# Kernel optimization log

Hardware: AMD Instinct MI355X
Metric: run time of the kernel (lower is better)

## Reference

```python
import jax, jax.numpy as jnp
import numpy as np

H = 12          # num_attention_heads
D = 768         # hidden_size
R = 4           # channel_shrink_ratio
DH = D // H     # 64, attention_head_size
DL = D // R     # 192, layout hidden size
DHL = DH // R   # 16, layout head size
NEG = jnp.finfo(jnp.float32).min


def setup_inputs() -> dict:
    key = jax.random.key(0)
    ks = jax.random.split(key, 16)
    B, S = 8, 1024
    s = 0.02
    inp = {
        "hidden_states": jax.random.normal(ks[0], (B, S, D), jnp.float32),
        "layout_hidden_states": jax.random.normal(ks[1], (B, S, DL), jnp.float32),
        "attention_mask": jnp.ones((B, S), jnp.float32),
        "Wq": jax.random.normal(ks[2], (D, D), jnp.float32) * s,
        "bq": jnp.zeros((D,), jnp.float32),
        "Wk": jax.random.normal(ks[3], (D, D), jnp.float32) * s,
        "bk": jnp.zeros((D,), jnp.float32),
        "Wv": jax.random.normal(ks[4], (D, D), jnp.float32) * s,
        "bv": jnp.zeros((D,), jnp.float32),
        "Wlq": jax.random.normal(ks[5], (DL, DL), jnp.float32) * s,
        "blq": jnp.zeros((DL,), jnp.float32),
        "Wlk": jax.random.normal(ks[6], (DL, DL), jnp.float32) * s,
        "blk": jnp.zeros((DL,), jnp.float32),
        "Wlv": jax.random.normal(ks[7], (DL, DL), jnp.float32) * s,
        "blv": jnp.zeros((DL,), jnp.float32),
    }
    return inp


def _heads(x, hd):
    # [B,S,H*hd] -> [B,H,S,hd]
    B, S, _ = x.shape
    return x.reshape(B, S, H, hd).transpose(0, 2, 1, 3)


def reference(hidden_states, layout_hidden_states, attention_mask,
              Wq, bq, Wk, bk, Wv, bv, Wlq, blq, Wlk, blk, Wlv, blv):
    B, S, _ = hidden_states.shape
    q = _heads(hidden_states @ Wq.T + bq, DH)
    k = _heads(hidden_states @ Wk.T + bk, DH)
    v = _heads(hidden_states @ Wv.T + bv, DH)
    lq = _heads(layout_hidden_states @ Wlq.T + blq, DHL)
    lk = _heads(layout_hidden_states @ Wlk.T + blk, DHL)
    lv = _heads(layout_hidden_states @ Wlv.T + blv, DHL)

    scores = jnp.einsum('bhqd,bhkd->bhqk', q, k) / jnp.sqrt(jnp.float32(DH))
    lscores = jnp.einsum('bhqd,bhkd->bhqk', lq, lk) / jnp.sqrt(jnp.float32(DHL))
    fused = scores + lscores  # cross-added scores (same for both streams)

    bias = (1.0 - attention_mask)[:, None, None, :] * NEG  # [B,1,1,S]
    fused = fused + bias

    probs = jax.nn.softmax(fused, axis=-1)   # dropout disabled (p=0)

    ctx = jnp.einsum('bhqk,bhkd->bhqd', probs, v)
    ctx = ctx.transpose(0, 2, 1, 3).reshape(B, S, D)
    lctx = jnp.einsum('bhqk,bhkd->bhqd', probs, lv)
    lctx = lctx.transpose(0, 2, 1, 3).reshape(B, S, DL)
    return ctx, lctx, probs
```

## Files before the change

### kernel.cpp

```cpp
#include <hip/hip_runtime.h>

#define NH   12
#define SEQ  1024
#define NB   8
#define DCAT 96
#define DV   80

typedef __attribute__((ext_vector_type(8))) short  bf16x8;
typedef __attribute__((ext_vector_type(4))) float  f32x4;
typedef __attribute__((ext_vector_type(4))) unsigned short u16x4;

static __device__ __forceinline__ unsigned short f2bf(float x) {
    unsigned int u = __float_as_uint(x);
    u += 0x7fffu + ((u >> 16) & 1u);
    return (unsigned short)(u >> 16);
}
static __device__ __forceinline__ f32x4 fzero() {
    f32x4 z; z[0]=0.f; z[1]=0.f; z[2]=0.f; z[3]=0.f; return z;
}
static __device__ __forceinline__ unsigned int cvtpk(float lo, float hi) {
    unsigned int r;
    asm("v_cvt_pk_bf16_f32 %0, %1, %2" : "=v"(r) : "v"(lo), "v"(hi));
    return r;
}
// ... 34 lines not shown
    o[0] = f2bf(v[0]); o[1] = f2bf(v[1]); o[2] = f2bf(v[2]); o[3] = f2bf(v[3]);
    ((u16x4*)dst)[off] = o;
}

__global__ __launch_bounds__(256) void proj_gemm(
    const unsigned short* __restrict__ A,
    const unsigned short* __restrict__ Bw,
    const float* __restrict__ b0, const float* __restrict__ b1, const float* __restrict__ b2,
    unsigned short* __restrict__ Qc, unsigned short* __restrict__ Kc, unsigned short* __restrict__ VT,
    int K, int Ntot, int variant)
{
    __shared__ __align__(16) unsigned short As[4096];
    __shared__ __align__(16) unsigned short Bs[4096];
    const int tid = threadIdx.x, w = tid >> 6, lane = tid & 63;
    const int g = lane >> 4, c = lane & 15;
    const int m0 = blockIdx.x * 128, n0 = blockIdx.y * 128;
    const int wr = w >> 1, wc = w & 1;
    const int srow = lane >> 2, scol = (lane & 3) * 8;

    f32x4 acc[4][4];
    #pragma unroll
    for (int m = 0; m < 4; m++)
        #pragma unroll
        for (int n = 0; n < 4; n++) acc[m][n] = fzero();

    const int ch0 = w * 2, ch1 = w * 2 + 1;
    const size_t arow0 = (size_t)(m0 + ch0 * 16 + srow) * K + scol;
    const size_t arow1 = (size_t)(m0 + ch1 * 16 + srow) * K + scol;
    int bn0 = n0 + ch0 * 16 + srow; if (bn0 >= Ntot) bn0 = Ntot - 1;
    int bn1 = n0 + ch1 * 16 + srow; if (bn1 >= Ntot) bn1 = Ntot - 1;
    const size_t brow0 = (size_t)bn0 * K + scol;
    const size_t brow1 = (size_t)bn1 * K + scol;

    for (int k0 = 0; k0 < K; k0 += 32) {
        __syncthreads();
        GLDS16(A  + arow0 + k0, As + ch0 * 512);
        GLDS16(A  + arow1 + k0, As + ch1 * 512);
        GLDS16(Bw + brow0 + k0, Bs + ch0 * 512);
        GLDS16(Bw + brow1 + k0, Bs + ch1 * 512);
        __syncthreads();
        bf16x8 af[4], bfr[4];
        #pragma unroll
        for (int m = 0; m < 4; m++) af[m]  = *(const bf16x8*)&As[(wr*64 + m*16 + c)*32 + g*8];
        #pragma unroll
        for (int n = 0; n < 4; n++) bfr[n] = *(const bf16x8*)&Bs[(wc*64 + n*16 + c)*32 + g*8];
        #pragma unroll
        for (int m = 0; m < 4; m++)
            #pragma unroll
            for (int n = 0; n < 4; n++)
                acc[m][n] = __builtin_amdgcn_mfma_f32_16x16x32_bf16(af[m], bfr[n], acc[m][n], 0, 0, 0);
    }

    const int b_ = m0 >> 10;
    #pragma unroll
    for (int nf = 0; nf < 4; nf++) {
        int n = n0 + wc * 64 + nf * 16 + c;
        if (n >= Ntot) continue;
        int seg, nn;
        if (variant == 0) { seg = (n >= 1536) ? 2 : ((n >= 768) ? 1 : 0); nn = n - seg * 768; }
        else              { seg = (n >= 384)  ? 2 : ((n >= 192) ? 1 : 0); nn = n - seg * 192; }
        const float* bp = (seg == 0) ? b0 : ((seg == 1) ? b1 : b2);
        float bv = bp[nn];
        float scale = (seg == 0) ? (variant ? 0.25f : 0.125f) : 1.0f;
        int h, d;
        if (variant == 0) { h = nn >> 6; d = nn & 63; }
        else              { h = nn >> 4; d = 64 + (nn & 15); }
        #pragma unroll
        for (int m = 0; m < 4; m++) {
            int row = m0 + wr * 64 + m * 16 + 4 * g;
            int s = row & 1023;
            if (seg < 2) {
                unsigned short* dst = (seg == 0) ? Qc : Kc;
                size_t base = (size_t)(b_ * NH + h) * SEQ;
                #pragma unroll
                for (int r = 0; r < 4; r++) {
                    dst[(base + s + r) * DCAT + d] = f2bf((acc[m][nf][r] + bv) * scale);
                    if (variant == 1)
                        dst[(base + s + r) * DCAT + d + 16] = 0;
                }
            } else {
                u16x4 pk;
                #pragma unroll
                for (int r = 0; r < 4; r++) pk[r] = f2bf(acc[m][nf][r] + bv);
                *(u16x4*)&VT[((size_t)(b_ * NH + h) * DV + d) * SEQ + s] = pk;
            }
        }
    }
}

__global__ __launch_bounds__(256, 3) void attn_kernel(
    const unsigned short* __restrict__ Qc,
    const unsigned short* __restrict__ Kc,
    const unsigned short* __restrict__ VT,
    const float* __restrict__ mask,
    float* __restrict__ ctx,
    float* __restrict__ lctx,
    float* __restrict__ probs)
{
    __shared__ __align__(16) unsigned short Ks[2 * 6144];
    __shared__ __align__(16) unsigned short pbuf[4][32][36];

    const int tid = threadIdx.x, w = tid >> 6, lane = tid & 63;
    const int g = lane >> 4, c = lane & 15;

    const int bid = blockIdx.x;
    const int xc = bid & 7, j = bid >> 3;
    const int bh = xc + 8 * (j >> 3);
    const int qt = j & 7;
    const int b = bh / NH, h = bh % NH;
    const int qrb = qt * 128 + w * 32;
    const float NEGF = -3.4028234663852886e38f;

    bf16x8 qa0, qa1, qa2, qb0, qb1, qb2;
    {
        const unsigned short* qr0 = &Qc[((size_t)bh * SEQ + qrb + c) * DCAT + g * 8];
        qa0 = *(const bf16x8*)(qr0);
        qa1 = *(const bf16x8*)(qr0 + 32);
        qa2 = *(const bf16x8*)(qr0 + 64);
        const unsigned short* qr1 = qr0 + 16 * DCAT;
        qb0 = *(const bf16x8*)(qr1);
        qb1 = *(const bf16x8*)(qr1 + 32);
        qb2 = *(const bf16x8*)(qr1 + 64);
    }
    const unsigned short* Kb = Kc + (size_t)bh * SEQ * DCAT;
    const unsigned short* Vb = VT + (size_t)bh * DV * SEQ;
    const float* mk = mask + b * SEQ;

    const int srow   = lane >> 2;
    const int schunk = (lane & 3) ^ ((lane >> 3) & 3);
    const int ssrc   = (w * 16 + srow) * DCAT + schunk * 8;
    unsigned short* sdst = &Ks[w * 512];

    const int slot8 = (g ^ ((c >> 1) & 3)) * 8;

    #pragma unroll
    for (int p = 0; p < 3; p++)
        GLDS16(Kb + ssrc + p * 32, sdst + p * 2048);
    __builtin_amdgcn_sched_barrier(0);
    WAITV("0");

    float sm0 = 0.f, sm1 = 0.f;
    for (int t = 0; t < 16; t++) {
        const int buf = t & 1;
        SBARRIER();
        if (t < 15) {
            const unsigned short* src = Kb + (t + 1) * 6144 + ssrc;
            unsigned short* dst = sdst + (buf ^ 1) * 6144;
            #pragma unroll
            for (int p = 0; p < 3; p++)
                GLDS16(src + p * 32, dst + p * 2048);
            __builtin_amdgcn_sched_barrier(0);
            WAITV("7");
        } else {
            WAITV("4");
        }
        #pragma unroll
        for (int ktl = 0; ktl < 4; ktl++) {
            const int rb = buf * 6144 + (ktl * 16 + c) * 32 + slot8;
            bf16x8 k0 = *(const bf16x8*)&Ks[rb];
            bf16x8 k1 = *(const bf16x8*)&Ks[rb + 2048];
            bf16x8 k2 = *(const bf16x8*)&Ks[rb + 4096];
            f32x4 m4 = *(const f32x4*)&mk[t * 64 + ktl * 16 + 4 * g];
            __builtin_amdgcn_s_setprio(1);
            f32x4 a0 = __builtin_amdgcn_mfma_f32_16x16x32_bf16(k0, qa0, fzero(), 0, 0, 0);
            f32x4 a1 = __builtin_amdgcn_mfma_f32_16x16x32_bf16(k1, qa1, fzero(), 0, 0, 0);
            f32x4 a2 = __builtin_amdgcn_mfma_f32_16x16x32_bf16(k2, qa2, fzero(), 0, 0, 0);
            f32x4 b0 = __builtin_amdgcn_mfma_f32_16x16x32_bf16(k0, qb0, fzero(), 0, 0, 0);
            f32x4 b1 = __builtin_amdgcn_mfma_f32_16x16x32_bf16(k1, qb1, fzero(), 0, 0, 0);
            f32x4 b2 = __builtin_amdgcn_mfma_f32_16x16x32_bf16(k2, qb2, fzero(), 0, 0, 0);
            __builtin_amdgcn_s_setprio(0);
            #pragma unroll
            for (int r = 0; r < 4; r++) {
                float bias = (1.0f - m4[r]) * NEGF;
                sm0 += __expf(a0[r] + a1[r] + a2[r] + bias);
                sm1 += __expf(b0[r] + b1[r] + b2[r] + bias);
            }
        }
    }
    sm0 += __shfl_xor(sm0, 16); sm0 += __shfl_xor(sm0, 32);
    sm1 += __shfl_xor(sm1, 16); sm1 += __shfl_xor(sm1, 32);
    const float rinv0 = 1.0f / fmaxf(sm0, 1e-38f);
    const float rinv1 = 1.0f / fmaxf(sm1, 1e-38f);

    f32x4 cacc0[5], cacc1[5];
    #pragma unroll
    for (int nf = 0; nf < 5; nf++) { cacc0[nf] = fzero(); cacc1[nf] = fzero(); }

    const size_t prow0 = ((size_t)bh * SEQ + qrb + c) * SEQ;
    const size_t prow1 = prow0 + 16 * SEQ;

    #pragma unroll
    for (int p = 0; p < 3; p++)
        GLDS16(Kb + ssrc + p * 32, sdst + p * 2048);
    __builtin_amdgcn_sched_barrier(0);
    WAITV("0");

    for (int t = 0; t < 16; t++) {
        const int buf = t & 1;
        SBARRIER();
        if (t < 15) {
            const unsigned short* src = Kb + (t + 1) * 6144 + ssrc;
            unsigned short* dst = sdst + (buf ^ 1) * 6144;
            #pragma unroll
            for (int p = 0; p < 3; p++)
                GLDS16(src + p * 32, dst + p * 2048);
            __builtin_amdgcn_sched_barrier(0);
            WAITV("25");
        } else {
            WAITV("22");
        }
        #pragma unroll
        for (int half = 0; half < 2; half++) {
            const int kp = t * 2 + half;
            bf16x8 vf0 = *(const bf16x8*)&Vb[(size_t)(0 * 16 + c) * SEQ + kp * 32 + g * 8];
            bf16x8 vf1 = *(const bf16x8*)&Vb[(size_t)(1 * 16 + c) * SEQ + kp * 32 + g * 8];
            bf16x8 vf2 = *(const bf16x8*)&Vb[(size_t)(2 * 16 + c) * SEQ + kp * 32 + g * 8];
            bf16x8 vf3 = *(const bf16x8*)&Vb[(size_t)(3 * 16 + c) * SEQ + kp * 32 + g * 8];
            bf16x8 vf4 = *(const bf16x8*)&Vb[(size_t)(4 * 16 + c) * SEQ + kp * 32 + g * 8];
            #pragma unroll
            for (int ph = 0; ph < 2; ph++) {
                const int ktl = half * 2 + ph;
                const int rb = buf * 6144 + (ktl * 16 + c) * 32 + slot8;
                bf16x8 k0 = *(const bf16x8*)&Ks[rb];
                bf16x8 k1 = *(const bf16x8*)&Ks[rb + 2048];
                bf16x8 k2 = *(const bf16x8*)&Ks[rb + 4096];
                f32x4 m4 = *(const f32x4*)&mk[t * 64 + ktl * 16 + 4 * g];
                __builtin_amdgcn_s_setprio(1);
                f32x4 a0 = __builtin_amdgcn_mfma_f32_16x16x32_bf16(k0, qa0, fzero(), 0, 0, 0);
                f32x4 a1 = __builtin_amdgcn_mfma_f32_16x16x32_bf16(k1, qa1, fzero(), 0, 0, 0);
                f32x4 a2 = __builtin_amdgcn_mfma_f32_16x16x32_bf16(k2, qa2, fzero(), 0, 0, 0);
                f32x4 b0 = __builtin_amdgcn_mfma_f32_16x16x32_bf16(k0, qb0, fzero(), 0, 0, 0);
                f32x4 b1 = __builtin_amdgcn_mfma_f32_16x16x32_bf16(k1, qb1, fzero(), 0, 0, 0);
                f32x4 b2 = __builtin_amdgcn_mfma_f32_16x16x32_bf16(k2, qb2, fzero(), 0, 0, 0);
                __builtin_amdgcn_s_setprio(0);
                f32x4 p0, p1;
                #pragma unroll
                for (int r = 0; r < 4; r++) {
                    float bias = (1.0f - m4[r]) * NEGF;
                    p0[r] = __expf(a0[r] + a1[r] + a2[r] + bias) * rinv0;
                    p1[r] = __expf(b0[r] + b1[r] + b2[r] + bias) * rinv1;
                }
                *(f32x4*)&probs[prow0 + (t * 64 + ktl * 16) + 4 * g] = p0;
                *(f32x4*)&probs[prow1 + (t * 64 + ktl * 16) + 4 * g] = p1;
                uint2 hh0, hh1;
                hh0.x = cvtpk(p0[0], p0[1]); hh0.y = cvtpk(p0[2], p0[3]);
                hh1.x = cvtpk(p1[0], p1[1]); hh1.y = cvtpk(p1[2], p1[3]);
                *(uint2*)&pbuf[w][c][ph * 16 + 4 * g]      = hh0;
                *(uint2*)&pbuf[w][16 + c][ph * 16 + 4 * g] = hh1;
            }
            bf16x8 pa0 = *(const bf16x8*)&pbuf[w][c][g * 8];
            bf16x8 pa1 = *(const bf16x8*)&pbuf[w][16 + c][g * 8];
            __builtin_amdgcn_s_setprio(1);
            cacc0[0] = __builtin_amdgcn_mfma_f32_16x16x32_bf16(pa0, vf0, cacc0[0], 0, 0, 0);
            cacc1[0] = __builtin_amdgcn_mfma_f32_16x16x32_bf16(pa1, vf0, cacc1[0], 0, 0, 0);
            cacc0[1] = __builtin_amdgcn_mfma_f32_16x16x32_bf16(pa0, vf1, cacc0[1], 0, 0, 0);
            cacc1[1] = __builtin_amdgcn_mfma_f32_16x16x32_bf16(pa1, vf1, cacc1[1], 0, 0, 0);
            cacc0[2] = __builtin_amdgcn_mfma_f32_16x16x32_bf16(pa0, vf2, cacc0[2], 0, 0, 0);
            cacc1[2] = __builtin_amdgcn_mfma_f32_16x16x32_bf16(pa1, vf2, cacc1[2], 0, 0, 0);
            cacc0[3] = __builtin_amdgcn_mfma_f32_16x16x32_bf16(pa0, vf3, cacc0[3], 0, 0, 0);
            cacc1[3] = __builtin_amdgcn_mfma_f32_16x16x32_bf16(pa1, vf3, cacc1[3], 0, 0, 0);
            cacc0[4] = __builtin_amdgcn_mfma_f32_16x16x32_bf16(pa0, vf4, cacc0[4], 0, 0, 0);
            cacc1[4] = __builtin_amdgcn_mfma_f32_16x16x32_bf16(pa1, vf4, cacc1[4], 0, 0, 0);
            __builtin_amdgcn_s_setprio(0);
        }
    }

    #pragma unroll
    for (int nf = 0; nf < 4; nf++)
        #pragma unroll
        for (int r = 0; r < 4; r++) {
            int q0 = qrb + 4 * g + r;
            ctx[((size_t)(b * SEQ + q0)) * 768 + h * 64 + nf * 16 + c] = cacc0[nf][r];
            ctx[((size_t)(b * SEQ + q0 + 16)) * 768 + h * 64 + nf * 16 + c] = cacc1[nf][r];
        }
    #pragma unroll
    for (int r = 0; r < 4; r++) {
        int q0 = qrb + 4 * g + r;
        lctx[((size_t)(b * SEQ + q0)) * 192 + h * 16 + c] = cacc0[4][r];
        lctx[((size_t)(b * SEQ + q0 + 16)) * 192 + h * 16 + c] = cacc1[4][r];
    }
}

extern "C" void kernel_launch(void* const* d_in, const int* in_sizes, int n_in,
                              void* d_out, int out_size, void* d_ws, size_t ws_size,
                              hipStream_t stream)
{
    const float* hs   = (const float*)d_in[0];
    const float* lhs  = (const float*)d_in[1];
    const float* mask = (const float*)d_in[2];
    const float* Wq   = (const float*)d_in[3];
    const float* bq   = (const float*)d_in[4];
    const float* Wk   = (const float*)d_in[5];
    const float* bk   = (const float*)d_in[6];
    const float* Wv   = (const float*)d_in[7];
    const float* bv   = (const float*)d_in[8];
    const float* Wlq  = (const float*)d_in[9];
    const float* blq  = (const float*)d_in[10];
    const float* Wlk  = (const float*)d_in[11];
    const float* blk_ = (const float*)d_in[12];
    const float* Wlv  = (const float*)d_in[13];
    const float* blv  = (const float*)d_in[14];

    float* out   = (float*)d_out;
    float* ctx   = out;
    float* lctx  = out + (size_t)NB * SEQ * 768;
    float* probs = out + (size_t)NB * SEQ * 768 + (size_t)NB * SEQ * 192;

    char* ws = (char*)d_ws;
    unsigned short* Qc     = (unsigned short*)(ws);
    unsigned short* Kc     = (unsigned short*)(ws + 18874368);
    unsigned short* VT     = (unsigned short*)(ws + 37748736);
    unsigned short* hid16  = (unsigned short*)(ws + 53477376);
    unsigned short* lay16  = (unsigned short*)(ws + 66060288);
    unsigned short* wqkv16 = (unsigned short*)(ws + 69206016);
    unsigned short* wl16   = (unsigned short*)(ws + 72744960);

    cvt_all<<<dim3(9516), dim3(256), 0, stream>>>(hs, lhs, Wq, Wk, Wv, Wlq, Wlk, Wlv,
                                                  hid16, lay16, wqkv16, wl16);

    proj_gemm<<<dim3(64, 18), dim3(256), 0, stream>>>(hid16, wqkv16, bq, bk, bv,
                                                      Qc, Kc, VT, 768, 2304, 0);
    proj_gemm<<<dim3(64, 5),  dim3(256), 0, stream>>>(lay16, wl16, blq, blk_, blv,
                                                      Qc, Kc, VT, 192, 576, 1);

    attn_kernel<<<dim3(768), dim3(256), 0, stream>>>(Qc, Kc, VT, mask, ctx, lctx, probs);
}
```

Before: 241.5 us.

## Triple-buffer K tiles in LDS and block V layout for contiguous loads

Converts the K-tile LDS staging from double to triple buffering, prefetching two tiles ahead with adjusted vmcnt waits, so global-to-LDS latency overlaps more compute. It also changes the V-transpose layout written by the projection kernel into 32-key blocks, so each V fragment load reads a contiguous 5 KB block instead of strided rows. The cost is larger shared memory per block (three 12 KB buffers), which may reduce occupancy under launch_bounds(256,3), plus an extra barrier before the second pass.

```diff
diff --git a/kernel.cpp b/kernel.cpp
--- a/kernel.cpp
+++ b/kernel.cpp
@@ -140,7 +140,8 @@
                 u16x4 pk;
                 #pragma unroll
                 for (int r = 0; r < 4; r++) pk[r] = f2bf(acc[m][nf][r] + bv);
-                *(u16x4*)&VT[((size_t)(b_ * NH + h) * DV + d) * SEQ + s] = pk;
+                int kb = s >> 5, ko = s & 31;
+                *(u16x4*)&VT[(((size_t)(b_ * NH + h) * 32 + kb) * DV + d) * 32 + ko] = pk;
             }
         }
     }
@@ -155,7 +156,7 @@
     float* __restrict__ lctx,
     float* __restrict__ probs)
 {
-    __shared__ __align__(16) unsigned short Ks[2 * 6144];
+    __shared__ __align__(16) unsigned short Ks[3 * 6144];
     __shared__ __align__(16) unsigned short pbuf[4][32][36];
 
     const int tid = threadIdx.x, w = tid >> 6, lane = tid & 63;
@@ -181,7 +182,7 @@
         qb2 = *(const bf16x8*)(qr1 + 64);
     }
     const unsigned short* Kb = Kc + (size_t)bh * SEQ * DCAT;
-    const unsigned short* Vb = VT + (size_t)bh * DV * SEQ;
+    const unsigned short* Vb = VT + (size_t)bh * 32 * DV * 32;
     const float* mk = mask + b * SEQ;
 
     const int srow   = lane >> 2;
@@ -192,93 +193,30 @@
     const int slot8 = (g ^ ((c >> 1) & 3)) * 8;
 
     #pragma unroll
-    for (int p = 0; p < 3; p++)
-        GLDS16(Kb + ssrc + p * 32, sdst + p * 2048);
+    for (int p = 0; p < 3; p++) GLDS16(Kb + 0 * 6144 + ssrc + p * 32, sdst + 0 * 6144 + p * 2048);
+    #pragma unroll
+    for (int p = 0; p < 3; p++) GLDS16(Kb + 1 * 6144 + ssrc + p * 32, sdst + 1 * 6144 + p * 2048);
     __builtin_amdgcn_sched_barrier(0);
-    WAITV("0");
 
     float sm0 = 0.f, sm1 = 0.f;
-    for (int t = 0; t < 16; t++) {
-        const int buf = t & 1;
-        SBARRIER();
-        if (t < 15) {
-            const unsigned short* src = Kb + (t + 1) * 6144 + ssrc;
-            unsigned short* dst = sdst + (buf ^ 1) * 6144;
+    {
+        int br = 0, bw = 2;
+        for (int t = 0; t < 16; t++) {
+            if (t == 0)       WAITV("3");
+            else if (t == 15) WAITV("4");
+            else              WAITV("7");
+            SBARRIER();
+            if (t < 14) {
+                const unsigned short* src = Kb + (t + 2) * 6144 + ssrc;
+                unsigned short* dst = sdst + bw * 6144;
+                #pragma unroll
+                for (int p = 0; p < 3; p++) GLDS16(src + p * 32, dst + p * 2048);
+                __builtin_amdgcn_sched_barrier(0);
+                bw = (bw == 2) ? 0 : bw + 1;
+            }
             #pragma unroll
-            for (int p = 0; p < 3; p++)
-                GLDS16(src + p * 32, dst + p * 2048);
-            __builtin_amdgcn_sched_barrier(0);
-            WAITV("7");
-        } else {
-            WAITV("4");
-        }
-        #pragma unroll
-        for (int ktl = 0; ktl < 4; ktl++) {
-            const int rb = buf * 6144 + (ktl * 16 + c) * 32 + slot8;
-            bf16x8 k0 = *(const bf16x8*)&Ks[rb];
-            bf16x8 k1 = *(const bf16x8*)&Ks[rb + 2048];
-            bf16x8 k2 = *(const bf16x8*)&Ks[rb + 4096];
-            f32x4 m4 = *(const f32x4*)&mk[t * 64 + ktl * 16 + 4 * g];
-            __builtin_amdgcn_s_setprio(1);
-            f32x4 a0 = __builtin_amdgcn_mfma_f32_16x16x32_bf16(k0, qa0, fzero(), 0, 0, 0);
-            f32x4 a1 = __builtin_amdgcn_mfma_f32_16x16x32_bf16(k1, qa1, fzero(), 0, 0, 0);
-            f32x4 a2 = __builtin_amdgcn_mfma_f32_16x16x32_bf16(k2, qa2, fzero(), 0, 0, 0);
-            f32x4 b0 = __builtin_amdgcn_mfma_f32_16x16x32_bf16(k0, qb0, fzero(), 0, 0, 0);
-            f32x4 b1 = __builtin_amdgcn_mfma_f32_16x16x32_bf16(k1, qb1, fzero(), 0, 0, 0);
-            f32x4 b2 = __builtin_amdgcn_mfma_f32_16x16x32_bf16(k2, qb2, fzero(), 0, 0, 0);
-            __builtin_amdgcn_s_setprio(0);
-            #pragma unroll
-            for (int r = 0; r < 4; r++) {
-                float bias = (1.0f - m4[r]) * NEGF;
-                sm0 += __expf(a0[r] + a1[r] + a2[r] + bias);
-                sm1 += __expf(b0[r] + b1[r] + b2[r] + bias);
-            }
-        }
-    }
-    sm0 += __shfl_xor(sm0, 16); sm0 += __shfl_xor(sm0, 32);
-    sm1 += __shfl_xor(sm1, 16); sm1 += __shfl_xor(sm1, 32);
-    const float rinv0 = 1.0f / fmaxf(sm0, 1e-38f);
-    const float rinv1 = 1.0f / fmaxf(sm1, 1e-38f);
-
-    f32x4 cacc0[5], cacc1[5];
-    #pragma unroll
-    for (int nf = 0; nf < 5; nf++) { cacc0[nf] = fzero(); cacc1[nf] = fzero(); }
-
-    const size_t prow0 = ((size_t)bh * SEQ + qrb + c) * SEQ;
-    const size_t prow1 = prow0 + 16 * SEQ;
-
-    #pragma unroll
-    for (int p = 0; p < 3; p++)
-        GLDS16(Kb + ssrc + p * 32, sdst + p * 2048);
-    __builtin_amdgcn_sched_barrier(0);
-    WAITV("0");
-
-    for (int t = 0; t < 16; t++) {
-        const int buf = t & 1;
-        SBARRIER();
-        if (t < 15) {
-            const unsigned short* src = Kb + (t + 1) * 6144 + ssrc;
-            unsigned short* dst = sdst + (buf ^ 1) * 6144;
-            #pragma unroll
-            for (int p = 0; p < 3; p++)
-                GLDS16(src + p * 32, dst + p * 2048);
-            __builtin_amdgcn_sched_barrier(0);
-            WAITV("25");
-        } else {
-            WAITV("22");
-        }
-        #pragma unroll
-        for (int half = 0; half < 2; half++) {
-            const int kp = t * 2 + half;
-            bf16x8 vf0 = *(const bf16x8*)&Vb[(size_t)(0 * 16 + c) * SEQ + kp * 32 + g * 8];
-            bf16x8 vf1 = *(const bf16x8*)&Vb[(size_t)(1 * 16 + c) * SEQ + kp * 32 + g * 8];
-            bf16x8 vf2 = *(const bf16x8*)&Vb[(size_t)(2 * 16 + c) * SEQ + kp * 32 + g * 8];
-            bf16x8 vf3 = *(const bf16x8*)&Vb[(size_t)(3 * 16 + c) * SEQ + kp * 32 + g * 8];
-            bf16x8 vf4 = *(const bf16x8*)&Vb[(size_t)(4 * 16 + c) * SEQ + kp * 32 + g * 8];
-            #pragma unroll
-            for (int ph = 0; ph < 2; ph++) {
-                const int ktl = half * 2 + ph;
-                const int rb = buf * 6144 + (ktl * 16 + c) * 32 + slot8;
+            for (int ktl = 0; ktl < 4; ktl++) {
+                const int rb = br * 6144 + (ktl * 16 + c) * 32 + slot8;
                 bf16x8 k0 = *(const bf16x8*)&Ks[rb];
                 bf16x8 k1 = *(const bf16x8*)&Ks[rb + 2048];
                 bf16x8 k2 = *(const bf16x8*)&Ks[rb + 4096];
@@ -291,35 +229,106 @@
                 f32x4 b1 = __builtin_amdgcn_mfma_f32_16x16x32_bf16(k1, qb1, fzero(), 0, 0, 0);
                 f32x4 b2 = __builtin_amdgcn_mfma_f32_16x16x32_bf16(k2, qb2, fzero(), 0, 0, 0);
                 __builtin_amdgcn_s_setprio(0);
-                f32x4 p0, p1;
                 #pragma unroll
                 for (int r = 0; r < 4; r++) {
                     float bias = (1.0f - m4[r]) * NEGF;
-                    p0[r] = __expf(a0[r] + a1[r] + a2[r] + bias) * rinv0;
-                    p1[r] = __expf(b0[r] + b1[r] + b2[r] + bias) * rinv1;
+                    sm0 += __expf(a0[r] + a1[r] + a2[r] + bias);
+                    sm1 += __expf(b0[r] + b1[r] + b2[r] + bias);
                 }
-                *(f32x4*)&probs[prow0 + (t * 64 + ktl * 16) + 4 * g] = p0;
-                *(f32x4*)&probs[prow1 + (t * 64 + ktl * 16) + 4 * g] = p1;
-                uint2 hh0, hh1;
-                hh0.x = cvtpk(p0[0], p0[1]); hh0.y = cvtpk(p0[2], p0[3]);
-                hh1.x = cvtpk(p1[0], p1[1]); hh1.y = cvtpk(p1[2], p1[3]);
-                *(uint2*)&pbuf[w][c][ph * 16 + 4 * g]      = hh0;
-                *(uint2*)&pbuf[w][16 + c][ph * 16 + 4 * g] = hh1;
-            }
-            bf16x8 pa0 = *(const bf16x8*)&pbuf[w][c][g * 8];
-            bf16x8 pa1 = *(const bf16x8*)&pbuf[w][16 + c][g * 8];
-            __builtin_amdgcn_s_setprio(1);
-            cacc0[0] = __builtin_amdgcn_mfma_f32_16x16x32_bf16(pa0, vf0, cacc0[0], 0, 0, 0);
-            cacc1[0] = __builtin_amdgcn_mfma_f32_16x16x32_bf16(pa1, vf0, cacc1[0], 0, 0, 0);
-            cacc0[1] = __builtin_amdgcn_mfma_f32_16x16x32_bf16(pa0, vf1, cacc0[1], 0, 0, 0);
-            cacc1[1] = __builtin_amdgcn_mfma_f32_16x16x32_bf16(pa1, vf1, cacc1[1], 0, 0, 0);
-            cacc0[2] = __builtin_amdgcn_mfma_f32_16x16x32_bf16(pa0, vf2, cacc0[2], 0, 0, 0);
-            cacc1[2] = __builtin_amdgcn_mfma_f32_16x16x32_bf16(pa1, vf2, cacc1[2], 0, 0, 0);
-            cacc0[3] = __builtin_amdgcn_mfma_f32_16x16x32_bf16(pa0, vf3, cacc0[3], 0, 0, 0);
-            cacc1[3] = __builtin_amdgcn_mfma_f32_16x16x32_bf16(pa1, vf3, cacc1[3], 0, 0, 0);
-            cacc0[4] = __builtin_amdgcn_mfma_f32_16x16x32_bf16(pa0, vf4, cacc0[4], 0, 0, 0);
-            cacc1[4] = __builtin_amdgcn_mfma_f32_16x16x32_bf16(pa1, vf4, cacc1[4], 0, 0, 0);
-            __builtin_amdgcn_s_setprio(0);
+            }
+            br = (br == 2) ? 0 : br + 1;
+        }
+    }
+    sm0 += __shfl_xor(sm0, 16); sm0 += __shfl_xor(sm0, 32);
+    sm1 += __shfl_xor(sm1, 16); sm1 += __shfl_xor(sm1, 32);
+    const float rinv0 = 1.0f / fmaxf(sm0, 1e-38f);
+    const float rinv1 = 1.0f / fmaxf(sm1, 1e-38f);
+
+    f32x4 cacc0[5], cacc1[5];
+    #pragma unroll
+    for (int nf = 0; nf < 5; nf++) { cacc0[nf] = fzero(); cacc1[nf] = fzero(); }
+
+    const size_t prow0 = ((size_t)bh * SEQ + qrb + c) * SEQ;
+    const size_t prow1 = prow0 + 16 * SEQ;
+
+    SBARRIER();
+    #pragma unroll
+    for (int p = 0; p < 3; p++) GLDS16(Kb + 0 * 6144 + ssrc + p * 32, sdst + 0 * 6144 + p * 2048);
+    #pragma unroll
+    for (int p = 0; p < 3; p++) GLDS16(Kb + 1 * 6144 + ssrc + p * 32, sdst + 1 * 6144 + p * 2048);
+    __builtin_amdgcn_sched_barrier(0);
+
+    {
+        int br = 0, bw = 2;
+        for (int t = 0; t < 16; t++) {
+            if (t == 0)       WAITV("3");
+            else if (t == 15) WAITV("22");
+            else              WAITV("25");
+            SBARRIER();
+            if (t < 14) {
+                const unsigned short* src = Kb + (t + 2) * 6144 + ssrc;
+                unsigned short* dst = sdst + bw * 6144;
+                #pragma unroll
+                for (int p = 0; p < 3; p++) GLDS16(src + p * 32, dst + p * 2048);
+                __builtin_amdgcn_sched_barrier(0);
+                bw = (bw == 2) ? 0 : bw + 1;
+            }
+            #pragma unroll
+            for (int half = 0; half < 2; half++) {
+                const int kp = t * 2 + half;
+                const unsigned short* vbk = Vb + (size_t)kp * (DV * 32) + c * 32 + g * 8;
+                bf16x8 vf0 = *(const bf16x8*)(vbk);
+                bf16x8 vf1 = *(const bf16x8*)(vbk + 16 * 32);
+                bf16x8 vf2 = *(const bf16x8*)(vbk + 32 * 32);
+                bf16x8 vf3 = *(const bf16x8*)(vbk + 48 * 32);
+                bf16x8 vf4 = *(const bf16x8*)(vbk + 64 * 32);
+                #pragma unroll
+                for (int ph = 0; ph < 2; ph++) {
+                    const int ktl = half * 2 + ph;
+                    const int rb = br * 6144 + (ktl * 16 + c) * 32 + slot8;
+                    bf16x8 k0 = *(const bf16x8*)&Ks[rb];
+                    bf16x8 k1 = *(const bf16x8*)&Ks[rb + 2048];
+                    bf16x8 k2 = *(const bf16x8*)&Ks[rb + 4096];
+                    f32x4 m4 = *(const f32x4*)&mk[t * 64 + ktl * 16 + 4 * g];
+                    __builtin_amdgcn_s_setprio(1);
+                    f32x4 a0 = __builtin_amdgcn_mfma_f32_16x16x32_bf16(k0, qa0, fzero(), 0, 0, 0);
+                    f32x4 a1 = __builtin_amdgcn_mfma_f32_16x16x32_bf16(k1, qa1, fzero(), 0, 0, 0);
+                    f32x4 a2 = __builtin_amdgcn_mfma_f32_16x16x32_bf16(k2, qa2, fzero(), 0, 0, 0);
+                    f32x4 b0 = __builtin_amdgcn_mfma_f32_16x16x32_bf16(k0, qb0, fzero(), 0, 0, 0);
+                    f32x4 b1 = __builtin_amdgcn_mfma_f32_16x16x32_bf16(k1, qb1, fzero(), 0, 0, 0);
+                    f32x4 b2 = __builtin_amdgcn_mfma_f32_16x16x32_bf16(k2, qb2, fzero(), 0, 0, 0);
+                    __builtin_amdgcn_s_setprio(0);
+                    f32x4 p0, p1;
+                    #pragma unroll
+                    for (int r = 0; r < 4; r++) {
+                        float bias = (1.0f - m4[r]) * NEGF;
+                        p0[r] = __expf(a0[r] + a1[r] + a2[r] + bias) * rinv0;
+                        p1[r] = __expf(b0[r] + b1[r] + b2[r] + bias) * rinv1;
+                    }
+                    *(f32x4*)&probs[prow0 + (t * 64 + ktl * 16) + 4 * g] = p0;
+                    *(f32x4*)&probs[prow1 + (t * 64 + ktl * 16) + 4 * g] = p1;
+                    uint2 hh0, hh1;
+                    hh0.x = cvtpk(p0[0], p0[1]); hh0.y = cvtpk(p0[2], p0[3]);
+                    hh1.x = cvtpk(p1[0], p1[1]); hh1.y = cvtpk(p1[2], p1[3]);
+                    *(uint2*)&pbuf[w][c][ph * 16 + 4 * g]      = hh0;
+                    *(uint2*)&pbuf[w][16 + c][ph * 16 + 4 * g] = hh1;
+                }
+                bf16x8 pa0 = *(const bf16x8*)&pbuf[w][c][g * 8];
+                bf16x8 pa1 = *(const bf16x8*)&pbuf[w][16 + c][g * 8];
+                __builtin_amdgcn_s_setprio(1);
+                cacc0[0] = __builtin_amdgcn_mfma_f32_16x16x32_bf16(pa0, vf0, cacc0[0], 0, 0, 0);
+                cacc1[0] = __builtin_amdgcn_mfma_f32_16x16x32_bf16(pa1, vf0, cacc1[0], 0, 0, 0);
+                cacc0[1] = __builtin_amdgcn_mfma_f32_16x16x32_bf16(pa0, vf1, cacc0[1], 0, 0, 0);
+                cacc1[1] = __builtin_amdgcn_mfma_f32_16x16x32_bf16(pa1, vf1, cacc1[1], 0, 0, 0);
+                cacc0[2] = __builtin_amdgcn_mfma_f32_16x16x32_bf16(pa0, vf2, cacc0[2], 0, 0, 0);
+                cacc1[2] = __builtin_amdgcn_mfma_f32_16x16x32_bf16(pa1, vf2, cacc1[2], 0, 0, 0);
+                cacc0[3] = __builtin_amdgcn_mfma_f32_16x16x32_bf16(pa0, vf3, cacc0[3], 0, 0, 0);
+                cacc1[3] = __builtin_amdgcn_mfma_f32_16x16x32_bf16(pa1, vf3, cacc1[3], 0, 0, 0);
+                cacc0[4] = __builtin_amdgcn_mfma_f32_16x16x32_bf16(pa0, vf4, cacc0[4], 0, 0, 0);
+                cacc1[4] = __builtin_amdgcn_mfma_f32_16x16x32_bf16(pa1, vf4, cacc1[4], 0, 0, 0);
+                __builtin_amdgcn_s_setprio(0);
+            }
+            br = (br == 2) ? 0 : br + 1;
         }
     }
 
```

Result: slower. 251.7 us (+4.2%).

## Halve query rows per wave, double grid, block V^T layout, raise occupancy

Applied to the files above, without the earlier changes.

Each wave now handles 16 query rows instead of 32, so the attention grid doubles to 1536 blocks and launch bounds allow 5 blocks per CU. V^T is stored in 32-key blocks so each wave's V fragment loads are contiguous. The K pipeline waits are moved before the barrier with adjusted counts. This buys more parallelism and occupancy, but each K tile from LDS is reused by half as many query rows, so K traffic per unit of work doubles.

```diff
diff --git a/kernel.cpp b/kernel.cpp
--- a/kernel.cpp
+++ b/kernel.cpp
@@ -140,13 +140,14 @@
                 u16x4 pk;
                 #pragma unroll
                 for (int r = 0; r < 4; r++) pk[r] = f2bf(acc[m][nf][r] + bv);
-                *(u16x4*)&VT[((size_t)(b_ * NH + h) * DV + d) * SEQ + s] = pk;
+                int kb = s >> 5, ko = s & 31;
+                *(u16x4*)&VT[(((size_t)(b_ * NH + h) * 32 + kb) * DV + d) * 32 + ko] = pk;
             }
         }
     }
 }
 
-__global__ __launch_bounds__(256, 3) void attn_kernel(
+__global__ __launch_bounds__(256, 5) void attn_kernel(
     const unsigned short* __restrict__ Qc,
     const unsigned short* __restrict__ Kc,
     const unsigned short* __restrict__ VT,
@@ -156,32 +157,28 @@
     float* __restrict__ probs)
 {
     __shared__ __align__(16) unsigned short Ks[2 * 6144];
-    __shared__ __align__(16) unsigned short pbuf[4][32][36];
+    __shared__ __align__(16) unsigned short pbuf[4][16][36];
 
     const int tid = threadIdx.x, w = tid >> 6, lane = tid & 63;
     const int g = lane >> 4, c = lane & 15;
 
     const int bid = blockIdx.x;
     const int xc = bid & 7, j = bid >> 3;
-    const int bh = xc + 8 * (j >> 3);
-    const int qt = j & 7;
+    const int bh = xc + 8 * (j >> 4);
+    const int qt = j & 15;
     const int b = bh / NH, h = bh % NH;
-    const int qrb = qt * 128 + w * 32;
+    const int qrb = qt * 64 + w * 16;
     const float NEGF = -3.4028234663852886e38f;
 
-    bf16x8 qa0, qa1, qa2, qb0, qb1, qb2;
+    bf16x8 qa0, qa1, qa2;
     {
         const unsigned short* qr0 = &Qc[((size_t)bh * SEQ + qrb + c) * DCAT + g * 8];
         qa0 = *(const bf16x8*)(qr0);
         qa1 = *(const bf16x8*)(qr0 + 32);
         qa2 = *(const bf16x8*)(qr0 + 64);
-        const unsigned short* qr1 = qr0 + 16 * DCAT;
-        qb0 = *(const bf16x8*)(qr1);
-        qb1 = *(const bf16x8*)(qr1 + 32);
-        qb2 = *(const bf16x8*)(qr1 + 64);
     }
     const unsigned short* Kb = Kc + (size_t)bh * SEQ * DCAT;
-    const unsigned short* Vb = VT + (size_t)bh * DV * SEQ;
+    const unsigned short* Vb = VT + (size_t)bh * 32 * DV * 32;
     const float* mk = mask + b * SEQ;
 
     const int srow   = lane >> 2;
@@ -192,25 +189,21 @@
     const int slot8 = (g ^ ((c >> 1) & 3)) * 8;
 
     #pragma unroll
-    for (int p = 0; p < 3; p++)
-        GLDS16(Kb + ssrc + p * 32, sdst + p * 2048);
+    for (int p = 0; p < 3; p++) GLDS16(Kb + ssrc + p * 32, sdst + p * 2048);
     __builtin_amdgcn_sched_barrier(0);
-    WAITV("0");
-
-    float sm0 = 0.f, sm1 = 0.f;
+
+    float sm0 = 0.f;
     for (int t = 0; t < 16; t++) {
         const int buf = t & 1;
+        if (t == 0) WAITV("0");
+        else        WAITV("4");
         SBARRIER();
         if (t < 15) {
             const unsigned short* src = Kb + (t + 1) * 6144 + ssrc;
             unsigned short* dst = sdst + (buf ^ 1) * 6144;
             #pragma unroll
-            for (int p = 0; p < 3; p++)
-                GLDS16(src + p * 32, dst + p * 2048);
+            for (int p = 0; p < 3; p++) GLDS16(src + p * 32, dst + p * 2048);
             __builtin_amdgcn_sched_barrier(0);
-            WAITV("7");
-        } else {
-            WAITV("4");
         }
         #pragma unroll
         for (int ktl = 0; ktl < 4; ktl++) {
@@ -223,58 +216,49 @@
             f32x4 a0 = __builtin_amdgcn_mfma_f32_16x16x32_bf16(k0, qa0, fzero(), 0, 0, 0);
             f32x4 a1 = __builtin_amdgcn_mfma_f32_16x16x32_bf16(k1, qa1, fzero(), 0, 0, 0);
             f32x4 a2 = __builtin_amdgcn_mfma_f32_16x16x32_bf16(k2, qa2, fzero(), 0, 0, 0);
-            f32x4 b0 = __builtin_amdgcn_mfma_f32_16x16x32_bf16(k0, qb0, fzero(), 0, 0, 0);
-            f32x4 b1 = __builtin_amdgcn_mfma_f32_16x16x32_bf16(k1, qb1, fzero(), 0, 0, 0);
-            f32x4 b2 = __builtin_amdgcn_mfma_f32_16x16x32_bf16(k2, qb2, fzero(), 0, 0, 0);
             __builtin_amdgcn_s_setprio(0);
             #pragma unroll
             for (int r = 0; r < 4; r++) {
                 float bias = (1.0f - m4[r]) * NEGF;
                 sm0 += __expf(a0[r] + a1[r] + a2[r] + bias);
-                sm1 += __expf(b0[r] + b1[r] + b2[r] + bias);
             }
         }
     }
     sm0 += __shfl_xor(sm0, 16); sm0 += __shfl_xor(sm0, 32);
-    sm1 += __shfl_xor(sm1, 16); sm1 += __shfl_xor(sm1, 32);
     const float rinv0 = 1.0f / fmaxf(sm0, 1e-38f);
-    const float rinv1 = 1.0f / fmaxf(sm1, 1e-38f);
-
-    f32x4 cacc0[5], cacc1[5];
-    #pragma unroll
-    for (int nf = 0; nf < 5; nf++) { cacc0[nf] = fzero(); cacc1[nf] = fzero(); }
+
+    f32x4 cacc[5];
+    #pragma unroll
+    for (int nf = 0; nf < 5; nf++) cacc[nf] = fzero();
 
     const size_t prow0 = ((size_t)bh * SEQ + qrb + c) * SEQ;
-    const size_t prow1 = prow0 + 16 * SEQ;
-
-    #pragma unroll
-    for (int p = 0; p < 3; p++)
-        GLDS16(Kb + ssrc + p * 32, sdst + p * 2048);
+
+    SBARRIER();
+    #pragma unroll
+    for (int p = 0; p < 3; p++) GLDS16(Kb + ssrc + p * 32, sdst + p * 2048);
     __builtin_amdgcn_sched_barrier(0);
-    WAITV("0");
 
     for (int t = 0; t < 16; t++) {
         const int buf = t & 1;
+        if (t == 0) WAITV("0");
+        else        WAITV("18");
         SBARRIER();
         if (t < 15) {
             const unsigned short* src = Kb + (t + 1) * 6144 + ssrc;
             unsigned short* dst = sdst + (buf ^ 1) * 6144;
             #pragma unroll
-            for (int p = 0; p < 3; p++)
-                GLDS16(src + p * 32, dst + p * 2048);
+            for (int p = 0; p < 3; p++) GLDS16(src + p * 32, dst + p * 2048);
             __builtin_amdgcn_sched_barrier(0);
-            WAITV("25");
-        } else {
-            WAITV("22");
         }
         #pragma unroll
         for (int half = 0; half < 2; half++) {
             const int kp = t * 2 + half;
-            bf16x8 vf0 = *(const bf16x8*)&Vb[(size_t)(0 * 16 + c) * SEQ + kp * 32 + g * 8];
-            bf16x8 vf1 = *(const bf16x8*)&Vb[(size_t)(1 * 16 + c) * SEQ + kp * 32 + g * 8];
-            bf16x8 vf2 = *(const bf16x8*)&Vb[(size_t)(2 * 16 + c) * SEQ + kp * 32 + g * 8];
-            bf16x8 vf3 = *(const bf16x8*)&Vb[(size_t)(3 * 16 + c) * SEQ + kp * 32 + g * 8];
-            bf16x8 vf4 = *(const bf16x8*)&Vb[(size_t)(4 * 16 + c) * SEQ + kp * 32 + g * 8];
+            const unsigned short* vbk = Vb + (size_t)kp * (DV * 32) + c * 32 + g * 8;
+            bf16x8 vf0 = *(const bf16x8*)(vbk);
+            bf16x8 vf1 = *(const bf16x8*)(vbk + 16 * 32);
+            bf16x8 vf2 = *(const bf16x8*)(vbk + 32 * 32);
+            bf16x8 vf3 = *(const bf16x8*)(vbk + 48 * 32);
+            bf16x8 vf4 = *(const bf16x8*)(vbk + 64 * 32);
             #pragma unroll
             for (int ph = 0; ph < 2; ph++) {
                 const int ktl = half * 2 + ph;
@@ -287,38 +271,25 @@
                 f32x4 a0 = __builtin_amdgcn_mfma_f32_16x16x32_bf16(k0, qa0, fzero(), 0, 0, 0);
                 f32x4 a1 = __builtin_amdgcn_mfma_f32_16x16x32_bf16(k1, qa1, fzero(), 0, 0, 0);
                 f32x4 a2 = __builtin_amdgcn_mfma_f32_16x16x32_bf16(k2, qa2, fzero(), 0, 0, 0);
-                f32x4 b0 = __builtin_amdgcn_mfma_f32_16x16x32_bf16(k0, qb0, fzero(), 0, 0, 0);
-                f32x4 b1 = __builtin_amdgcn_mfma_f32_16x16x32_bf16(k1, qb1, fzero(), 0, 0, 0);
-                f32x4 b2 = __builtin_amdgcn_mfma_f32_16x16x32_bf16(k2, qb2, fzero(), 0, 0, 0);
                 __builtin_amdgcn_s_setprio(0);
-                f32x4 p0, p1;
+                f32x4 p0;
                 #pragma unroll
                 for (int r = 0; r < 4; r++) {
                     float bias = (1.0f - m4[r]) * NEGF;
                     p0[r] = __expf(a0[r] + a1[r] + a2[r] + bias) * rinv0;
-                    p1[r] = __expf(b0[r] + b1[r] + b2[r] + bias) * rinv1;
                 }
                 *(f32x4*)&probs[prow0 + (t * 64 + ktl * 16) + 4 * g] = p0;
-                *(f32x4*)&probs[prow1 + (t * 64 + ktl * 16) + 4 * g] = p1;
-                uint2 hh0, hh1;
+                uint2 hh0;
                 hh0.x = cvtpk(p0[0], p0[1]); hh0.y = cvtpk(p0[2], p0[3]);
-                hh1.x = cvtpk(p1[0], p1[1]); hh1.y = cvtpk(p1[2], p1[3]);
-                *(uint2*)&pbuf[w][c][ph * 16 + 4 * g]      = hh0;
-                *(uint2*)&pbuf[w][16 + c][ph * 16 + 4 * g] = hh1;
+                *(uint2*)&pbuf[w][c][ph * 16 + 4 * g] = hh0;
             }
             bf16x8 pa0 = *(const bf16x8*)&pbuf[w][c][g * 8];
-            bf16x8 pa1 = *(const bf16x8*)&pbuf[w][16 + c][g * 8];
             __builtin_amdgcn_s_setprio(1);
-            cacc0[0] = __builtin_amdgcn_mfma_f32_16x16x32_bf16(pa0, vf0, cacc0[0], 0, 0, 0);
-            cacc1[0] = __builtin_amdgcn_mfma_f32_16x16x32_bf16(pa1, vf0, cacc1[0], 0, 0, 0);
-            cacc0[1] = __builtin_amdgcn_mfma_f32_16x16x32_bf16(pa0, vf1, cacc0[1], 0, 0, 0);
-            cacc1[1] = __builtin_amdgcn_mfma_f32_16x16x32_bf16(pa1, vf1, cacc1[1], 0, 0, 0);
-            cacc0[2] = __builtin_amdgcn_mfma_f32_16x16x32_bf16(pa0, vf2, cacc0[2], 0, 0, 0);
-            cacc1[2] = __builtin_amdgcn_mfma_f32_16x16x32_bf16(pa1, vf2, cacc1[2], 0, 0, 0);
-            cacc0[3] = __builtin_amdgcn_mfma_f32_16x16x32_bf16(pa0, vf3, cacc0[3], 0, 0, 0);
-            cacc1[3] = __builtin_amdgcn_mfma_f32_16x16x32_bf16(pa1, vf3, cacc1[3], 0, 0, 0);
-            cacc0[4] = __builtin_amdgcn_mfma_f32_16x16x32_bf16(pa0, vf4, cacc0[4], 0, 0, 0);
-            cacc1[4] = __builtin_amdgcn_mfma_f32_16x16x32_bf16(pa1, vf4, cacc1[4], 0, 0, 0);
+            cacc[0] = __builtin_amdgcn_mfma_f32_16x16x32_bf16(pa0, vf0, cacc[0], 0, 0, 0);
+            cacc[1] = __builtin_amdgcn_mfma_f32_16x16x32_bf16(pa0, vf1, cacc[1], 0, 0, 0);
+            cacc[2] = __builtin_amdgcn_mfma_f32_16x16x32_bf16(pa0, vf2, cacc[2], 0, 0, 0);
+            cacc[3] = __builtin_amdgcn_mfma_f32_16x16x32_bf16(pa0, vf3, cacc[3], 0, 0, 0);
+            cacc[4] = __builtin_amdgcn_mfma_f32_16x16x32_bf16(pa0, vf4, cacc[4], 0, 0, 0);
             __builtin_amdgcn_s_setprio(0);
         }
     }
@@ -328,14 +299,12 @@
         #pragma unroll
         for (int r = 0; r < 4; r++) {
             int q0 = qrb + 4 * g + r;
-            ctx[((size_t)(b * SEQ + q0)) * 768 + h * 64 + nf * 16 + c] = cacc0[nf][r];
-            ctx[((size_t)(b * SEQ + q0 + 16)) * 768 + h * 64 + nf * 16 + c] = cacc1[nf][r];
+            ctx[((size_t)(b * SEQ + q0)) * 768 + h * 64 + nf * 16 + c] = cacc[nf][r];
         }
     #pragma unroll
     for (int r = 0; r < 4; r++) {
         int q0 = qrb + 4 * g + r;
-        lctx[((size_t)(b * SEQ + q0)) * 192 + h * 16 + c] = cacc0[4][r];
-        lctx[((size_t)(b * SEQ + q0 + 16)) * 192 + h * 16 + c] = cacc1[4][r];
+        lctx[((size_t)(b * SEQ + q0)) * 192 + h * 16 + c] = cacc[4][r];
     }
 }
 
@@ -381,5 +350,5 @@
     proj_gemm<<<dim3(64, 5),  dim3(256), 0, stream>>>(lay16, wl16, blq, blk_, blv,
                                                       Qc, Kc, VT, 192, 576, 1);
 
-    attn_kernel<<<dim3(768), dim3(256), 0, stream>>>(Qc, Kc, VT, mask, ctx, lctx, probs);
-}
+    attn_kernel<<<dim3(1536), dim3(256), 0, stream>>>(Qc, Kc, VT, mask, ctx, lctx, probs);
+}
```

Result: slower. 292.9 us (+21.3%).

## Stage V tiles through LDS with K in blocked layout and finer pipeline

Applied to the files above, without the earlier changes.

The projection kernel now writes V^T in a blocked layout of 32-key chunks, so each chunk of V for a head is contiguous. In the second attention pass, K and V tiles for 32 keys are loaded together into double-buffered shared memory with async global-to-LDS copies, replacing per-lane direct global V loads. The pass now runs 32 smaller steps instead of 16, and the wait counters move ahead of the barrier. The intent is to cut scattered global V traffic and hide its latency, at the cost of more barriers per key sweep.

```diff
diff --git a/kernel.cpp b/kernel.cpp
--- a/kernel.cpp
+++ b/kernel.cpp
@@ -140,7 +140,8 @@
                 u16x4 pk;
                 #pragma unroll
                 for (int r = 0; r < 4; r++) pk[r] = f2bf(acc[m][nf][r] + bv);
-                *(u16x4*)&VT[((size_t)(b_ * NH + h) * DV + d) * SEQ + s] = pk;
+                int kb = s >> 5, ko = s & 31;
+                *(u16x4*)&VT[(((size_t)(b_ * NH + h) * 32 + kb) * DV + d) * 32 + ko] = pk;
             }
         }
     }
@@ -181,36 +182,32 @@
         qb2 = *(const bf16x8*)(qr1 + 64);
     }
     const unsigned short* Kb = Kc + (size_t)bh * SEQ * DCAT;
-    const unsigned short* Vb = VT + (size_t)bh * DV * SEQ;
+    const unsigned short* Vb = VT + (size_t)bh * 32 * DV * 32;
     const float* mk = mask + b * SEQ;
+
+    const int slot8 = (g ^ ((c >> 1) & 3)) * 8;
 
     const int srow   = lane >> 2;
     const int schunk = (lane & 3) ^ ((lane >> 3) & 3);
-    const int ssrc   = (w * 16 + srow) * DCAT + schunk * 8;
-    unsigned short* sdst = &Ks[w * 512];
-
-    const int slot8 = (g ^ ((c >> 1) & 3)) * 8;
-
-    #pragma unroll
-    for (int p = 0; p < 3; p++)
-        GLDS16(Kb + ssrc + p * 32, sdst + p * 2048);
+    const int ssrcA  = (w * 16 + srow) * DCAT + schunk * 8;
+    unsigned short* sdstA = &Ks[w * 512];
+
+    #pragma unroll
+    for (int p = 0; p < 3; p++) GLDS16(Kb + ssrcA + p * 32, sdstA + p * 2048);
     __builtin_amdgcn_sched_barrier(0);
-    WAITV("0");
 
     float sm0 = 0.f, sm1 = 0.f;
     for (int t = 0; t < 16; t++) {
         const int buf = t & 1;
+        if (t == 0) WAITV("0");
+        else        WAITV("4");
         SBARRIER();
         if (t < 15) {
-            const unsigned short* src = Kb + (t + 1) * 6144 + ssrc;
-            unsigned short* dst = sdst + (buf ^ 1) * 6144;
-            #pragma unroll
-            for (int p = 0; p < 3; p++)
-                GLDS16(src + p * 32, dst + p * 2048);
+            const unsigned short* src = Kb + (t + 1) * 6144 + ssrcA;
+            unsigned short* dst = sdstA + (buf ^ 1) * 6144;
+            #pragma unroll
+            for (int p = 0; p < 3; p++) GLDS16(src + p * 32, dst + p * 2048);
             __builtin_amdgcn_sched_barrier(0);
-            WAITV("7");
-        } else {
-            WAITV("4");
         }
         #pragma unroll
         for (int ktl = 0; ktl < 4; ktl++) {
@@ -240,6 +237,28 @@
     const float rinv0 = 1.0f / fmaxf(sm0, 1e-38f);
     const float rinv1 = 1.0f / fmaxf(sm1, 1e-38f);
 
+    const unsigned short* gsrc[3]; int gstep[3];
+    #pragma unroll
+    for (int r = 0; r < 3; r++) {
+        const int m = tid + 256 * r;
+        if (m < 384) {
+            int p = m >> 7, row = (m >> 2) & 31, jj = m & 3;
+            int jx = jj ^ ((row >> 1) & 3);
+            gsrc[r]  = Kb + row * DCAT + p * 32 + jx * 8;
+            gstep[r] = 32 * DCAT;
+        } else if (m < 704) {
+            int mv = m - 384;
+            int df = mv >> 6, cc = (mv >> 2) & 15, jj = mv & 3;
+            int jx = jj ^ ((cc >> 1) & 3);
+            gsrc[r]  = Vb + (df * 16 + cc) * 32 + jx * 8;
+            gstep[r] = DV * 32;
+        } else {
+            gsrc[r]  = Vb;
+            gstep[r] = 0;
+        }
+    }
+    const int dub = w * 512;
+
     f32x4 cacc0[5], cacc1[5];
     #pragma unroll
     for (int nf = 0; nf < 5; nf++) { cacc0[nf] = fzero(); cacc1[nf] = fzero(); }
@@ -247,80 +266,74 @@
     const size_t prow0 = ((size_t)bh * SEQ + qrb + c) * SEQ;
     const size_t prow1 = prow0 + 16 * SEQ;
 
-    #pragma unroll
-    for (int p = 0; p < 3; p++)
-        GLDS16(Kb + ssrc + p * 32, sdst + p * 2048);
+    SBARRIER();
+    #pragma unroll
+    for (int r = 0; r < 3; r++)
+        GLDS16(gsrc[r], Ks + r * 2048 + dub);
     __builtin_amdgcn_sched_barrier(0);
-    WAITV("0");
-
-    for (int t = 0; t < 16; t++) {
+
+    for (int t = 0; t < 32; t++) {
         const int buf = t & 1;
+        if (t == 0) WAITV("0");
+        else        WAITV("6");
         SBARRIER();
-        if (t < 15) {
-            const unsigned short* src = Kb + (t + 1) * 6144 + ssrc;
-            unsigned short* dst = sdst + (buf ^ 1) * 6144;
-            #pragma unroll
-            for (int p = 0; p < 3; p++)
-                GLDS16(src + p * 32, dst + p * 2048);
+        if (t < 31) {
+            #pragma unroll
+            for (int r = 0; r < 3; r++)
+                GLDS16(gsrc[r] + (t + 1) * gstep[r], Ks + (buf ^ 1) * 6144 + r * 2048 + dub);
             __builtin_amdgcn_sched_barrier(0);
-            WAITV("25");
-        } else {
-            WAITV("22");
-        }
-        #pragma unroll
-        for (int half = 0; half < 2; half++) {
-            const int kp = t * 2 + half;
-            bf16x8 vf0 = *(const bf16x8*)&Vb[(size_t)(0 * 16 + c) * SEQ + kp * 32 + g * 8];
-            bf16x8 vf1 = *(const bf16x8*)&Vb[(size_t)(1 * 16 + c) * SEQ + kp * 32 + g * 8];
-            bf16x8 vf2 = *(const bf16x8*)&Vb[(size_t)(2 * 16 + c) * SEQ + kp * 32 + g * 8];
-            bf16x8 vf3 = *(const bf16x8*)&Vb[(size_t)(3 * 16 + c) * SEQ + kp * 32 + g * 8];
-            bf16x8 vf4 = *(const bf16x8*)&Vb[(size_t)(4 * 16 + c) * SEQ + kp * 32 + g * 8];
-            #pragma unroll
-            for (int ph = 0; ph < 2; ph++) {
-                const int ktl = half * 2 + ph;
-                const int rb = buf * 6144 + (ktl * 16 + c) * 32 + slot8;
-                bf16x8 k0 = *(const bf16x8*)&Ks[rb];
-                bf16x8 k1 = *(const bf16x8*)&Ks[rb + 2048];
-                bf16x8 k2 = *(const bf16x8*)&Ks[rb + 4096];
-                f32x4 m4 = *(const f32x4*)&mk[t * 64 + ktl * 16 + 4 * g];
-                __builtin_amdgcn_s_setprio(1);
-                f32x4 a0 = __builtin_amdgcn_mfma_f32_16x16x32_bf16(k0, qa0, fzero(), 0, 0, 0);
-                f32x4 a1 = __builtin_amdgcn_mfma_f32_16x16x32_bf16(k1, qa1, fzero(), 0, 0, 0);
-                f32x4 a2 = __builtin_amdgcn_mfma_f32_16x16x32_bf16(k2, qa2, fzero(), 0, 0, 0);
-                f32x4 b0 = __builtin_amdgcn_mfma_f32_16x16x32_bf16(k0, qb0, fzero(), 0, 0, 0);
-                f32x4 b1 = __builtin_amdgcn_mfma_f32_16x16x32_bf16(k1, qb1, fzero(), 0, 0, 0);
-                f32x4 b2 = __builtin_amdgcn_mfma_f32_16x16x32_bf16(k2, qb2, fzero(), 0, 0, 0);
-                __builtin_amdgcn_s_setprio(0);
-                f32x4 p0, p1;
-                #pragma unroll
-                for (int r = 0; r < 4; r++) {
-                    float bias = (1.0f - m4[r]) * NEGF;
-                    p0[r] = __expf(a0[r] + a1[r] + a2[r] + bias) * rinv0;
-                    p1[r] = __expf(b0[r] + b1[r] + b2[r] + bias) * rinv1;
-                }
-                *(f32x4*)&probs[prow0 + (t * 64 + ktl * 16) + 4 * g] = p0;
-                *(f32x4*)&probs[prow1 + (t * 64 + ktl * 16) + 4 * g] = p1;
-                uint2 hh0, hh1;
-                hh0.x = cvtpk(p0[0], p0[1]); hh0.y = cvtpk(p0[2], p0[3]);
-                hh1.x = cvtpk(p1[0], p1[1]); hh1.y = cvtpk(p1[2], p1[3]);
-                *(uint2*)&pbuf[w][c][ph * 16 + 4 * g]      = hh0;
-                *(uint2*)&pbuf[w][16 + c][ph * 16 + 4 * g] = hh1;
+        }
+        const int vb0 = buf * 6144 + 3072 + c * 32 + slot8;
+        bf16x8 vf0 = *(const bf16x8*)&Ks[vb0];
+        bf16x8 vf1 = *(const bf16x8*)&Ks[vb0 + 512];
+        bf16x8 vf2 = *(const bf16x8*)&Ks[vb0 + 1024];
+        bf16x8 vf3 = *(const bf16x8*)&Ks[vb0 + 1536];
+        bf16x8 vf4 = *(const bf16x8*)&Ks[vb0 + 2048];
+
+        #pragma unroll
+        for (int ktl = 0; ktl < 2; ktl++) {
+            const int rb = buf * 6144 + (ktl * 16 + c) * 32 + slot8;
+            bf16x8 k0 = *(const bf16x8*)&Ks[rb];
+            bf16x8 k1 = *(const bf16x8*)&Ks[rb + 1024];
+            bf16x8 k2 = *(const bf16x8*)&Ks[rb + 2048];
+            f32x4 m4 = *(const f32x4*)&mk[t * 32 + ktl * 16 + 4 * g];
+            __builtin_amdgcn_s_setprio(1);
+            f32x4 a0 = __builtin_amdgcn_mfma_f32_16x16x32_bf16(k0, qa0, fzero(), 0, 0, 0);
+            f32x4 a1 = __builtin_amdgcn_mfma_f32_16x16x32_bf16(k1, qa1, fzero(), 0, 0, 0);
+            f32x4 a2 = __builtin_amdgcn_mfma_f32_16x16x32_bf16(k2, qa2, fzero(), 0, 0, 0);
+            f32x4 b0 = __builtin_amdgcn_mfma_f32_16x16x32_bf16(k0, qb0, fzero(), 0, 0, 0);
+            f32x4 b1 = __builtin_amdgcn_mfma_f32_16x16x32_bf16(k1, qb1, fzero(), 0, 0, 0);
+            f32x4 b2 = __builtin_amdgcn_mfma_f32_16x16x32_bf16(k2, qb2, fzero(), 0, 0, 0);
+            __builtin_amdgcn_s_setprio(0);
+            f32x4 p0, p1;
+            #pragma unroll
+            for (int r = 0; r < 4; r++) {
+                float bias = (1.0f - m4[r]) * NEGF;
+                p0[r] = __expf(a0[r] + a1[r] + a2[r] + bias) * rinv0;
+                p1[r] = __expf(b0[r] + b1[r] + b2[r] + bias) * rinv1;
             }
-            bf16x8 pa0 = *(const bf16x8*)&pbuf[w][c][g * 8];
-            bf16x8 pa1 = *(const bf16x8*)&pbuf[w][16 + c][g * 8];
-            __builtin_amdgcn_s_setprio(1);
-            cacc0[0] = __builtin_amdgcn_mfma_f32_16x16x32_bf16(pa0, vf0, cacc0[0], 0, 0, 0);
-            cacc1[0] = __builtin_amdgcn_mfma_f32_16x16x32_bf16(pa1, vf0, cacc1[0], 0, 0, 0);
-            cacc0[1] = __builtin_amdgcn_mfma_f32_16x16x32_bf16(pa0, vf1, cacc0[1], 0, 0, 0);
-            cacc1[1] = __builtin_amdgcn_mfma_f32_16x16x32_bf16(pa1, vf1, cacc1[1], 0, 0, 0);
-            cacc0[2] = __builtin_amdgcn_mfma_f32_16x16x32_bf16(pa0, vf2, cacc0[2], 0, 0, 0);
-            cacc1[2] = __builtin_amdgcn_mfma_f32_16x16x32_bf16(pa1, vf2, cacc1[2], 0, 0, 0);
-            cacc0[3] = __builtin_amdgcn_mfma_f32_16x16x32_bf16(pa0, vf3, cacc0[3], 0, 0, 0);
-            cacc1[3] = __builtin_amdgcn_mfma_f32_16x16x32_bf16(pa1, vf3, cacc1[3], 0, 0, 0);
-            cacc0[4] = __builtin_amdgcn_mfma_f32_16x16x32_bf16(pa0, vf4, cacc0[4], 0, 0, 0);
-            cacc1[4] = __builtin_amdgcn_mfma_f32_16x16x32_bf16(pa1, vf4, cacc1[4], 0, 0, 0);
-            __builtin_amdgcn_s_setprio(0);
-        }
+            *(f32x4*)&probs[prow0 + (t * 32 + ktl * 16) + 4 * g] = p0;
+            *(f32x4*)&probs[prow1 + (t * 32 + ktl * 16) + 4 * g] = p1;
+            uint2 hh0, hh1;
+            hh0.x = cvtpk(p0[0], p0[1]); hh0.y = cvtpk(p0[2], p0[3]);
+            hh1.x = cvtpk(p1[0], p1[1]); hh1.y = cvtpk(p1[2], p1[3]);
+            *(uint2*)&pbuf[w][c][ktl * 16 + 4 * g]      = hh0;
+            *(uint2*)&pbuf[w][16 + c][ktl * 16 + 4 * g] = hh1;
+        }
+        bf16x8 pa0 = *(const bf16x8*)&pbuf[w][c][g * 8];
+        bf16x8 pa1 = *(const bf16x8*)&pbuf[w][16 + c][g * 8];
+        __builtin_amdgcn_s_setprio(1);
+        cacc0[0] = __builtin_amdgcn_mfma_f32_16x16x32_bf16(pa0, vf0, cacc0[0], 0, 0, 0);
+        cacc1[0] = __builtin_amdgcn_mfma_f32_16x16x32_bf16(pa1, vf0, cacc1[0], 0, 0, 0);
+        cacc0[1] = __builtin_amdgcn_mfma_f32_16x16x32_bf16(pa0, vf1, cacc0[1], 0, 0, 0);
+        cacc1[1] = __builtin_amdgcn_mfma_f32_16x16x32_bf16(pa1, vf1, cacc1[1], 0, 0, 0);
+        cacc0[2] = __builtin_amdgcn_mfma_f32_16x16x32_bf16(pa0, vf2, cacc0[2], 0, 0, 0);
+        cacc1[2] = __builtin_amdgcn_mfma_f32_16x16x32_bf16(pa1, vf2, cacc1[2], 0, 0, 0);
+        cacc0[3] = __builtin_amdgcn_mfma_f32_16x16x32_bf16(pa0, vf3, cacc0[3], 0, 0, 0);
+        cacc1[3] = __builtin_amdgcn_mfma_f32_16x16x32_bf16(pa1, vf3, cacc1[3], 0, 0, 0);
+        cacc0[4] = __builtin_amdgcn_mfma_f32_16x16x32_bf16(pa0, vf4, cacc0[4], 0, 0, 0);
+        cacc1[4] = __builtin_amdgcn_mfma_f32_16x16x32_bf16(pa1, vf4, cacc1[4], 0, 0, 0);
+        __builtin_amdgcn_s_setprio(0);
     }
 
     #pragma unroll
```

New measurement: 250.2 us. 3.6% more time.
